# Kernel tuning notes

Hardware: AMD Instinct MI355X
Metric: run time of the kernel (lower is better)

Reference implementation:

```python
import jax, jax.numpy as jnp
import numpy as np

HIDDEN_DIM = 256
ATTN_DIM = 256
N_TOKENS = 32768
N_CODES = 4096
RMS_EPS = 1e-5


def _rms_norm(x, weight):
    # fp32 variance like the torch module, eps=1e-5, elementwise affine (no bias)
    var = jnp.mean(x.astype(jnp.float32) ** 2, axis=-1, keepdims=True)
    x = x * jax.lax.rsqrt(var + RMS_EPS)
    return x * weight


def setup_inputs() -> dict:
    key = jax.random.key(0)
    ks = jax.random.split(key, 10)
    s_in = 1.0 / np.sqrt(HIDDEN_DIM).astype(np.float32)
    return {
        "hidden_states": jax.random.normal(ks[0], (N_TOKENS, HIDDEN_DIM), jnp.float32),
        "codebook_hidden_states": jax.random.normal(ks[1], (N_CODES, HIDDEN_DIM), jnp.float32),
        # Linear weights stored as [in, out] (y = x @ W + b)
        "wq": jax.random.normal(ks[2], (HIDDEN_DIM, ATTN_DIM), jnp.float32) * s_in,
        "bq": jnp.zeros((ATTN_DIM,), jnp.float32),
        "wk": jax.random.normal(ks[3], (HIDDEN_DIM, ATTN_DIM), jnp.float32) * s_in,
        "bk": jnp.zeros((ATTN_DIM,), jnp.float32),
        "wv": jax.random.normal(ks[4], (HIDDEN_DIM, HIDDEN_DIM), jnp.float32) * s_in,
        "bv": jnp.zeros((HIDDEN_DIM,), jnp.float32),
        "gq": jnp.ones((ATTN_DIM,), jnp.float32),  # RMSNorm weight for q
        "gk": jnp.ones((ATTN_DIM,), jnp.float32),  # RMSNorm weight for k
    }


def reference(hidden_states, codebook_hidden_states, wq, bq, wk, bk, wv, bv, gq, gk):
    # projections (small-d GEMMs)
    q = hidden_states @ wq + bq                     # [NT, A]
    k = codebook_hidden_states @ wk + bk            # [N, A]
    v = codebook_hidden_states @ wv + bv            # [N, C]

    scale = 1.0 / jnp.sqrt(jnp.asarray(q.shape[-1], q.dtype))
    q = _rms_norm(q, gq)
    k = _rms_norm(k, gk)

    logits = jnp.einsum("bd,nd->bn", q, k) * scale  # [NT, N]
    soft_one_hot = jax.nn.softmax(logits, axis=1)
    idx_N = jnp.argmax(logits, axis=1)              # argmax(softmax) == argmax(logits)
    hard_one_hot = jax.nn.one_hot(idx_N, logits.shape[1], dtype=logits.dtype)
    # straight-through estimator
    one_hot = hard_one_hot - jax.lax.stop_gradient(soft_one_hot) + soft_one_hot

    z_q = jnp.einsum("bn,nd->bd", one_hot, v)       # [NT, C]
    z_q_2 = jnp.einsum("bn,nd->bd", hard_one_hot, v)
    return (logits, idx_N[:, None], z_q, z_q_2)
```

## Files before the change

### kernel.cpp

```cpp
#include <hip/hip_runtime.h>
#include <hip/hip_bf16.h>


#define NTOK 32768
#define NCODE 4096
#define DIM 256

typedef __bf16 bf16x8 __attribute__((ext_vector_type(8)));
typedef float f32x4 __attribute__((ext_vector_type(4)));

__device__ __forceinline__ void nt_store4(const float4& v, float* p) {
    f32x4 w; w[0] = v.x; w[1] = v.y; w[2] = v.z; w[3] = v.w;
    __builtin_nontemporal_store(w, (f32x4*)p);
}

__global__ __launch_bounds__(256, 2)
void gemm_fused(const float* __restrict__ hs, const float* __restrict__ cb,
                const float* __restrict__ wq, const float* __restrict__ bq,
                const float* __restrict__ wk, const float* __restrict__ bk,
                const float* __restrict__ wv, const float* __restrict__ bv,
                float* __restrict__ qf, float* __restrict__ kf, float* __restrict__ vf)
{
    __shared__ __align__(16) float Xs[32][132];
    __shared__ __align__(16) float Ws[32][132];
    const int t  = threadIdx.x;
    const int tm = t >> 4;
    const int tn = t & 15;

    const int bx = blockIdx.x;
    const float* X; const float* W; const float* bias; float* Y; int mb;
    if (bx < 32)      { X = cb; W = wk; bias = bk; Y = kf; mb = bx * 128; }
    else if (bx < 64) { X = cb; W = wv; bias = bv; Y = vf; mb = (bx - 32) * 128; }
    else              { X = hs; W = wq; bias = bq; Y = qf; mb = (bx - 64) * 128; }
    const int nb = blockIdx.y * 128;

    float acc[8][8];
    #pragma unroll
    for (int i = 0; i < 8; ++i)
        #pragma unroll
        for (int j = 0; j < 8; ++j) acc[i][j] = 0.f;

    const int sxm = t >> 1;
    const int sxh = (t & 1) * 16;
    const int swk = t >> 3;
    const int swc = (t & 7) * 16;

    for (int kb = 0; kb < 256; kb += 32) {
        float4 xv[4], wv4[4];
        #pragma unroll
        for (int i = 0; i < 4; ++i) {
            xv[i]  = *(const float4*)&X[(size_t)(mb + sxm) * 256 + kb + sxh + 4 * i];
            wv4[i] = *(const float4*)&W[(size_t)(kb + swk) * 256 + nb + swc + 4 * i];
        }
        __syncthreads();
        #pragma unroll
        for (int i = 0; i < 4; ++i) {
            Xs[sxh + 4*i + 0][sxm] = xv[i].x;
            Xs[sxh + 4*i + 1][sxm] = xv[i].y;
            Xs[sxh + 4*i + 2][sxm] = xv[i].z;
            Xs[sxh + 4*i + 3][sxm] = xv[i].w;
            *(float4*)&Ws[swk][swc + 4*i] = wv4[i];
        }
        __syncthreads();
        #pragma unroll 8
        for (int kk = 0; kk < 32; ++kk) {
            float4 a0 = *(const float4*)&Xs[kk][tm*8];
            float4 a1 = *(const float4*)&Xs[kk][tm*8 + 4];
            float4 b0 = *(const float4*)&Ws[kk][tn*8];
            float4 b1 = *(const float4*)&Ws[kk][tn*8 + 4];
            float av[8] = {a0.x,a0.y,a0.z,a0.w,a1.x,a1.y,a1.z,a1.w};
            float bw[8] = {b0.x,b0.y,b0.z,b0.w,b1.x,b1.y,b1.z,b1.w};
            #pragma unroll
            for (int i = 0; i < 8; ++i)
                #pragma unroll
                for (int j = 0; j < 8; ++j)
                    acc[i][j] = fmaf(av[i], bw[j], acc[i][j]);
        }
    }

    float4 bb0 = *(const float4*)&bias[nb + tn*8];
    float4 bb1 = *(const float4*)&bias[nb + tn*8 + 4];
    float bb[8] = {bb0.x,bb0.y,bb0.z,bb0.w,bb1.x,bb1.y,bb1.z,bb1.w};
    #pragma unroll
    for (int i = 0; i < 8; ++i) {
        const size_t row = (size_t)(mb + tm*8 + i);
        float4 o0 = {acc[i][0]+bb[0], acc[i][1]+bb[1], acc[i][2]+bb[2], acc[i][3]+bb[3]};
        float4 o1 = {acc[i][4]+bb[4], acc[i][5]+bb[5], acc[i][6]+bb[6], acc[i][7]+bb[7]};
        *(float4*)&Y[row*256 + nb + tn*8]     = o0;
        *(float4*)&Y[row*256 + nb + tn*8 + 4] = o1;
    }
}

__global__ __launch_bounds__(256)
void rmsnorm_fused(float* __restrict__ kf, float* __restrict__ qf,
                   const float* __restrict__ gk, const float* __restrict__ gq,
                   __hip_bfloat16* __restrict__ kb, __hip_bfloat16* __restrict__ qb)
{
    const int b = blockIdx.x;
    float* X; const float* g; __hip_bfloat16* Xb; size_t row;
    if (b < 1024) { X = kf; g = gk; Xb = kb; row = (size_t)b * 4 + (threadIdx.x >> 6); }
    else { X = qf; g = gq; Xb = qb; row = (size_t)(b - 1024) * 4 + (threadIdx.x >> 6); }

    const int lane = threadIdx.x & 63;
    float4 x = *(const float4*)&X[row*256 + lane*4];
    float ssq = fmaf(x.x, x.x, fmaf(x.y, x.y, fmaf(x.z, x.z, x.w * x.w)));
    #pragma unroll
    for (int o = 1; o < 64; o <<= 1) ssq += __shfl_xor(ssq, o, 64);
    const float r = 1.0f / sqrtf(ssq * (1.0f/256.0f) + 1e-5f);
    float4 gg = *(const float4*)&g[lane*4];
    float y0 = (x.x*r)*gg.x, y1 = (x.y*r)*gg.y, y2 = (x.z*r)*gg.z, y3 = (x.w*r)*gg.w;
    float4 y = {y0, y1, y2, y3};
    *(float4*)&X[row*256 + lane*4] = y;
    __hip_bfloat16 h0 = __float2bfloat16(y0), h1 = __float2bfloat16(y1);
    __hip_bfloat16 h2 = __float2bfloat16(y2), h3 = __float2bfloat16(y3);
    ushort4 p;
    p.x = *(unsigned short*)&h0; p.y = *(unsigned short*)&h1;
    p.z = *(unsigned short*)&h2; p.w = *(unsigned short*)&h3;
    ((ushort4*)Xb)[row*64 + lane] = p;
}

__device__ __forceinline__ void load_lds16(const void* g, void* l) {
    __builtin_amdgcn_global_load_lds((const __attribute__((address_space(1))) unsigned int*)g,
                                     (__attribute__((address_space(3))) unsigned int*)l, 16, 0, 0);
}

__global__ __launch_bounds__(256, 4)
void mfma_logits(const __hip_bfloat16* __restrict__ Qb, const __hip_bfloat16* __restrict__ Kb,
                 float* __restrict__ Out, float* __restrict__ Tmax)
{
    __shared__ __align__(16) char smem[33792];
    __hip_bfloat16* Asm = (__hip_bfloat16*)smem;
    __hip_bfloat16* Bsm = (__hip_bfloat16*)(smem + 16384);
    float*          Eps = (float*)smem;
    float*          Pmax = (float*)(smem + 32768);

    const int t    = threadIdx.x;
    const int lane = t & 63;
    const int w    = t >> 6;
    const int wm = w >> 1, wn = w & 1;

    const int bid = blockIdx.x;
    const int xcd = bid & 7;
    const int cid = bid >> 3;
    const int mb  = (xcd * 32 + (cid & 31)) * 128;
    const int ctl = cid >> 5;
    const int nb  = ctl * 128;

    const int grow   = t >> 3;
    const int gslot  = (t & 7) ^ ((t >> 3) & 7);
    const __hip_bfloat16* gA = Qb + (size_t)(mb + grow) * 256 + gslot * 8;
    const __hip_bfloat16* gB = Kb + (size_t)(nb + grow) * 256 + gslot * 8;
    __hip_bfloat16* lA = &Asm[w * 512];
    __hip_bfloat16* lB = &Bsm[w * 512];

    const int fr = lane & 15;
    const int kq = lane >> 4;
    const int rswz = lane & 7;
    const int ra0 = (wm * 64 + fr) * 64;
    const int rb0 = (wn * 64 + fr) * 64;

    f32x4 acc[4][4];
    #pragma unroll
    for (int mi = 0; mi < 4; ++mi)
        #pragma unroll
        for (int ni = 0; ni < 4; ++ni) {
            acc[mi][ni][0] = 0.f; acc[mi][ni][1] = 0.f;
            acc[mi][ni][2] = 0.f; acc[mi][ni][3] = 0.f;
        }

    for (int ks = 0; ks < 4; ++ks) {
        const int k0 = ks * 64;
        #pragma unroll
        for (int i = 0; i < 4; ++i) {
            load_lds16(gA + (size_t)i * 32 * 256 + k0, lA + i * 2048);
            load_lds16(gB + (size_t)i * 32 * 256 + k0, lB + i * 2048);
        }
        __syncthreads();

        #pragma unroll
        for (int kh = 0; kh < 2; ++kh) {
            bf16x8 af[4], bg[4];
            #pragma unroll
            for (int mi = 0; mi < 4; ++mi)
                af[mi] = *(const bf16x8*)&Asm[ra0 + mi*16*64 + (((kh<<2) + kq) ^ rswz) * 8];
            #pragma unroll
            for (int ni = 0; ni < 4; ++ni)
                bg[ni] = *(const bf16x8*)&Bsm[rb0 + ni*16*64 + (((kh<<2) + kq) ^ rswz) * 8];
            #pragma unroll
            for (int mi = 0; mi < 4; ++mi)
                #pragma unroll
                for (int ni = 0; ni < 4; ++ni)
                    acc[mi][ni] = __builtin_amdgcn_mfma_f32_16x16x32_bf16(
                        af[mi], bg[ni], acc[mi][ni], 0, 0, 0);
        }
        __syncthreads();
    }

    #pragma unroll
    for (int mi = 0; mi < 4; ++mi)
        #pragma unroll
        for (int j = 0; j < 4; ++j) {
            float mx = fmaxf(fmaxf(acc[mi][0][j], acc[mi][1][j]),
                             fmaxf(acc[mi][2][j], acc[mi][3][j]));
            #pragma unroll
            for (int o = 1; o < 16; o <<= 1) mx = fmaxf(mx, __shfl_xor(mx, o, 64));
            if ((lane & 15) == 0)
                Pmax[(wm*64 + mi*16 + (lane>>4)*4 + j)*2 + wn] = mx;
        }

    const int cr = (lane >> 4) * 4;
    const int cc = lane & 15;
    #pragma unroll
    for (int c = 0; c < 2; ++c) {
        if (wm == c) {
            #pragma unroll
            for (int mi = 0; mi < 4; ++mi)
                #pragma unroll
                for (int ni = 0; ni < 4; ++ni) {
                    const int lrow = mi*16 + cr;
                    const int lcol = wn*64 + ni*16 + cc;
                    #pragma unroll
                    for (int j = 0; j < 4; ++j) {
                        float v = acc[mi][ni][j] * 0.0625f;
                        v = fminf(fmaxf(v, -16.0f), 16.0f);
                        Eps[(lrow + j) * 128 + lcol] = v;
                    }
                }
        }
        __syncthreads();
        #pragma unroll
        for (int it = 0; it < 8; ++it) {
            const int p   = it * 1024 + t * 4;
            const int row = p >> 7;
            const int col = p & 127;
            float4 v = *(const float4*)&Eps[p];
            nt_store4(v, &Out[(size_t)(mb + c*64 + row) * 4096 + nb + col]);
        }
        __syncthreads();
    }

    if (t < 128) {
        float raw = fmaxf(Pmax[t*2], Pmax[t*2 + 1]);
        float v = raw * 0.0625f;
        v = fminf(fmaxf(v, -16.0f), 16.0f);
        Tmax[(size_t)(mb + t) * 32 + ctl] = v;
    }
}

__device__ __forceinline__ float dot256_f32(const float* __restrict__ a, const float* __restrict__ b)
{
    float s0 = 0.f, s1 = 0.f, s2 = 0.f, s3 = 0.f;
    #pragma unroll 8
    for (int j = 0; j < 64; ++j) {
        float4 x = ((const float4*)a)[j];
        float4 y = ((const float4*)b)[j];
        s0 = fmaf(x.x, y.x, s0);
        s1 = fmaf(x.y, y.y, s1);
        s2 = fmaf(x.z, y.z, s2);
        s3 = fmaf(x.w, y.w, s3);
    }
    return (s0 + s1) + (s2 + s3);
}

__global__ __launch_bounds__(256)
void refine_argmax_fast(const float* __restrict__ L, const float* __restrict__ Tmax,
                        const float* __restrict__ Qf, const float* __restrict__ Kf,
                        const float* __restrict__ Vf, float* __restrict__ OutIdx,
                        float* __restrict__ Zq, float* __restrict__ Zq2)
{
    __shared__ int cnt[4];
    __shared__ int list[4][256];
    const int lane = threadIdx.x & 63;
    const int w    = threadIdx.x >> 6;
    const size_t row = (size_t)blockIdx.x * 4 + w;

    float tm = (lane < 32) ? Tmax[row * 32 + lane] : -INFINITY;
    float gmax = tm;
    #pragma unroll
    for (int o = 1; o < 64; o <<= 1) gmax = fmaxf(gmax, __shfl_xor(gmax, o, 64));
    const float thr = gmax - 0.5f;

    if (lane == 0) cnt[w] = 0;
    __syncthreads();

    unsigned long long cmask = __ballot(tm >= thr);
    while (cmask) {
        const int tile = __ffsll(cmask) - 1;
        cmask &= cmask - 1;
        const float2 v2 = *(const float2*)&L[row * 4096 + tile * 128 + lane * 2];
        if (v2.x >= thr) {
            int slot = atomicAdd(&cnt[w], 1);
            if (slot < 256) list[w][slot] = tile*128 + lane*2;
        }
        if (v2.y >= thr) {
            int slot = atomicAdd(&cnt[w], 1);
            if (slot < 256) list[w][slot] = tile*128 + lane*2 + 1;
        }
    }
    __syncthreads();

    int m = cnt[w]; if (m > 256) m = 256;
    float bv = -INFINITY;
    int   bi = 0x7fffffff;
    const float* qrow = Qf + row * 256;
    for (int base = 0; base < m; base += 64) {
        const int ci = base + lane;
        if (ci < m) {
            const int c = list[w][ci];
            float rv = dot256_f32(qrow, Kf + (size_t)c * 256) * 0.0625f;
            if (rv > bv || (rv == bv && c < bi)) { bv = rv; bi = c; }
        }
    }
    #pragma unroll
    for (int o = 1; o < 64; o <<= 1) {
        float ov = __shfl_xor(bv, o, 64);
        int   oi = __shfl_xor(bi, o, 64);
        if (ov > bv || (ov == bv && oi < bi)) { bv = ov; bi = oi; }
    }

    if (bi < 0) bi = 0;
    if (bi > 4095) bi = 4095;

    if (lane == 0) __builtin_nontemporal_store((float)bi, &OutIdx[row]);

    float4 vv = ((const float4*)(Vf + (size_t)bi * 256))[lane];
    nt_store4(vv, (float*)&((float4*)Zq)[row*64 + lane]);
    nt_store4(vv, (float*)&((float4*)Zq2)[row*64 + lane]);
}

extern "C" void kernel_launch(void* const* d_in, const int* in_sizes, int n_in,
                              void* d_out, int out_size, void* d_ws, size_t ws_size,
                              hipStream_t stream)
{
    (void)in_sizes; (void)n_in; (void)out_size;
    const float* hs = (const float*)d_in[0];
    const float* cb = (const float*)d_in[1];
    const float* wq = (const float*)d_in[2];
    const float* bq = (const float*)d_in[3];
    const float* wk = (const float*)d_in[4];
    const float* bk = (const float*)d_in[5];
    const float* wv = (const float*)d_in[6];
    const float* bv = (const float*)d_in[7];
    const float* gq = (const float*)d_in[8];
    const float* gk = (const float*)d_in[9];
    float* out = (float*)d_out;

    if (ws_size < 31457280u) return;

    float* qf = out + 134250496ull;

    char* ws = (char*)d_ws;
    float* kf = (float*)ws;
    float* vf = (float*)(ws + 4194304);
    __hip_bfloat16* qb = (__hip_bfloat16*)(ws + 8388608);
    __hip_bfloat16* kb = (__hip_bfloat16*)(ws + 25165824);
    float* tmax = (float*)(ws + 27262976);

    gemm_fused<<<dim3(320, 2), 256, 0, stream>>>(hs, cb, wq, bq, wk, bk, wv, bv,
                                                 qf, kf, vf);
    rmsnorm_fused<<<9216, 256, 0, stream>>>(kf, qf, gk, gq, kb, qb);
    mfma_logits<<<8192, 256, 0, stream>>>(qb, kb, out, tmax);
    refine_argmax_fast<<<8192, 256, 0, stream>>>(out, tmax, qf, kf, vf,
        out + 134217728ull,
        out + 134250496ull,
        out + 142639104ull);
}
```

Before: 435.2 us.

## Double-buffer K-tiles in MFMA logits kernel to overlap global-to-LDS loads

The logits GEMM main loop now uses K-steps of 32 instead of 64, held in two LDS buffers. The next tile is issued with global_load_lds before computing on the current one, and explicit vmcnt waits plus raw barriers replace __syncthreads. The swizzle and read addressing change to match the narrower 32-wide rows. This aims to hide global load latency behind MFMA work, at the cost of twice as many barriers per tile and hand-tuned waitcnt logic that has to be correct.

```diff
diff --git a/kernel.cpp b/kernel.cpp
--- a/kernel.cpp
+++ b/kernel.cpp
@@ -129,10 +129,8 @@
                  float* __restrict__ Out, float* __restrict__ Tmax)
 {
     __shared__ __align__(16) char smem[33792];
-    __hip_bfloat16* Asm = (__hip_bfloat16*)smem;
-    __hip_bfloat16* Bsm = (__hip_bfloat16*)(smem + 16384);
-    float*          Eps = (float*)smem;
-    float*          Pmax = (float*)(smem + 32768);
+    float* Eps  = (float*)smem;
+    float* Pmax = (float*)(smem + 32768);
 
     const int t    = threadIdx.x;
     const int lane = t & 63;
@@ -146,18 +144,16 @@
     const int ctl = cid >> 5;
     const int nb  = ctl * 128;
 
-    const int grow   = t >> 3;
-    const int gslot  = (t & 7) ^ ((t >> 3) & 7);
-    const __hip_bfloat16* gA = Qb + (size_t)(mb + grow) * 256 + gslot * 8;
-    const __hip_bfloat16* gB = Kb + (size_t)(nb + grow) * 256 + gslot * 8;
-    __hip_bfloat16* lA = &Asm[w * 512];
-    __hip_bfloat16* lB = &Bsm[w * 512];
+    const int sr = w*16 + (lane >> 2);
+    const int sc = (lane & 3) ^ ((lane >> 2) & 3);
+    const __hip_bfloat16* gAr = Qb + (size_t)(mb + sr) * 256 + sc * 8;
+    const __hip_bfloat16* gBr = Kb + (size_t)(nb + sr) * 256 + sc * 8;
 
     const int fr = lane & 15;
     const int kq = lane >> 4;
-    const int rswz = lane & 7;
-    const int ra0 = (wm * 64 + fr) * 64;
-    const int rb0 = (wn * 64 + fr) * 64;
+    const int rdsw = (kq ^ (fr & 3)) * 8;
+    const int ra0 = (wm * 64 + fr) * 32;
+    const int rb0 = (wn * 64 + fr) * 32;
 
     f32x4 acc[4][4];
     #pragma unroll
@@ -168,32 +164,52 @@
             acc[mi][ni][2] = 0.f; acc[mi][ni][3] = 0.f;
         }
 
-    for (int ks = 0; ks < 4; ++ks) {
-        const int k0 = ks * 64;
-        #pragma unroll
-        for (int i = 0; i < 4; ++i) {
-            load_lds16(gA + (size_t)i * 32 * 256 + k0, lA + i * 2048);
-            load_lds16(gB + (size_t)i * 32 * 256 + k0, lB + i * 2048);
-        }
-        __syncthreads();
-
-        #pragma unroll
-        for (int kh = 0; kh < 2; ++kh) {
-            bf16x8 af[4], bg[4];
-            #pragma unroll
-            for (int mi = 0; mi < 4; ++mi)
-                af[mi] = *(const bf16x8*)&Asm[ra0 + mi*16*64 + (((kh<<2) + kq) ^ rswz) * 8];
+    {
+        char* dA = smem;
+        char* dB = smem + 8192;
+        load_lds16(gAr,             dA + w*1024);
+        load_lds16(gAr + 64*256,    dA + 4096 + w*1024);
+        load_lds16(gBr,             dB + w*1024);
+        load_lds16(gBr + 64*256,    dB + 4096 + w*1024);
+    }
+
+    #pragma unroll
+    for (int ks = 0; ks < 8; ++ks) {
+        char* curA = (ks & 1) ? (smem + 16384) : smem;
+        char* curB = (ks & 1) ? (smem + 24576) : (smem + 8192);
+        if (ks < 7) {
+            const int k0 = (ks + 1) * 32;
+            char* nxtA = (ks & 1) ? smem : (smem + 16384);
+            char* nxtB = (ks & 1) ? (smem + 8192) : (smem + 24576);
+            load_lds16(gAr + k0,          nxtA + w*1024);
+            load_lds16(gAr + 64*256 + k0, nxtA + 4096 + w*1024);
+            load_lds16(gBr + k0,          nxtB + w*1024);
+            load_lds16(gBr + 64*256 + k0, nxtB + 4096 + w*1024);
+            asm volatile("s_waitcnt vmcnt(4)" ::: "memory");
+        } else {
+            asm volatile("s_waitcnt vmcnt(0)" ::: "memory");
+        }
+        __builtin_amdgcn_s_barrier();
+
+        const __hip_bfloat16* A = (const __hip_bfloat16*)curA;
+        const __hip_bfloat16* B = (const __hip_bfloat16*)curB;
+        bf16x8 af[4], bg[4];
+        #pragma unroll
+        for (int mi = 0; mi < 4; ++mi)
+            af[mi] = *(const bf16x8*)&A[ra0 + mi*16*32 + rdsw];
+        #pragma unroll
+        for (int ni = 0; ni < 4; ++ni)
+            bg[ni] = *(const bf16x8*)&B[rb0 + ni*16*32 + rdsw];
+        #pragma unroll
+        for (int mi = 0; mi < 4; ++mi)
             #pragma unroll
             for (int ni = 0; ni < 4; ++ni)
-                bg[ni] = *(const bf16x8*)&Bsm[rb0 + ni*16*64 + (((kh<<2) + kq) ^ rswz) * 8];
-            #pragma unroll
-            for (int mi = 0; mi < 4; ++mi)
-                #pragma unroll
-                for (int ni = 0; ni < 4; ++ni)
-                    acc[mi][ni] = __builtin_amdgcn_mfma_f32_16x16x32_bf16(
-                        af[mi], bg[ni], acc[mi][ni], 0, 0, 0);
-        }
-        __syncthreads();
+                acc[mi][ni] = __builtin_amdgcn_mfma_f32_16x16x32_bf16(
+                    af[mi], bg[ni], acc[mi][ni], 0, 0, 0);
+
+        asm volatile("s_waitcnt lgkmcnt(0)" ::: "memory");
+        __builtin_amdgcn_sched_barrier(0);
+        __builtin_amdgcn_s_barrier();
     }
 
     #pragma unroll
```

Result: faster. 424.0 us (-2.6%).
